# Kernel optimization log

Measured on AMD Instinct MI355X. Metric: run time of the kernel, lower is better.

The kernel has to match this reference:

```python
import jax, jax.numpy as jnp
import numpy as np

# NOTE: the original source calls an undefined selective_scan_fn(x, delta, A_bar, B_bar, C)
# and returns y_proj(y). We implement the standard S6 diagonal selective scan it implies:
#   h_t = A_bar_t * h_{t-1} + B_bar_t * u_t   (elementwise over latent dim, h_0 = 0)
#   y_t = C_t * h_t
# with u = x_proj(x) (the only use of the otherwise-dangling x_proj in the source).

IN_CH = 96
OUT_CH = 96
LATENT = 256
BATCH, H, W = 2, 128, 128


def _linear(x, w, b):
    return x @ w.T + b


def _s6(x, xw, xb, bcw, bcb, dw, db, yw, yb):
    # x: [B, L, Cin]
    u = _linear(x, xw, xb)                      # [B, L, D]
    bc = _linear(x, bcw, bcb)                   # [B, L, 2D]
    delta = _linear(x, dw, db)                  # [B, L, D]
    Bm, Cm = jnp.split(bc, 2, axis=-1)
    A_bar = jnp.exp(-jax.nn.softplus(delta))    # in (0, 1)
    B_bar = (1.0 - A_bar) * Bm
    elems = (A_bar, B_bar * u)

    def combine(c1, c2):
        a1, b1 = c1
        a2, b2 = c2
        return (a1 * a2, a2 * b1 + b2)

    _, h = jax.lax.associative_scan(combine, elems, axis=1)  # parallel scan over L
    y = Cm * h
    return _linear(y, yw, yb)                   # [B, L, D]


def setup_inputs() -> dict:
    key = jax.random.key(0)
    ks = jax.random.split(key, 16)
    s = 0.02
    inp = {
        "x": jax.random.normal(ks[0], (BATCH, IN_CH, H, W), jnp.float32),
        # S6 params (shared across all 4 directional scans, as in the source)
        "xw": jax.random.normal(ks[1], (LATENT, IN_CH), jnp.float32) * s,
        "xb": jnp.zeros((LATENT,), jnp.float32),
        "bcw": jax.random.normal(ks[2], (2 * LATENT, IN_CH), jnp.float32) * s,
        "bcb": jnp.zeros((2 * LATENT,), jnp.float32),
        "dw": jax.random.normal(ks[3], (LATENT, IN_CH), jnp.float32) * s,
        "db": jnp.zeros((LATENT,), jnp.float32),
        "yw": jax.random.normal(ks[4], (LATENT, LATENT), jnp.float32) * s,
        "yb": jnp.zeros((LATENT,), jnp.float32),
        # CrossMerge params
        "mw": jax.random.normal(ks[5], (LATENT, 4 * LATENT), jnp.float32) * s,
        "mb": jnp.zeros((LATENT,), jnp.float32),
        "gw": jax.random.normal(ks[6], (LATENT, 4 * LATENT), jnp.float32) * s,
        "gb": jnp.zeros((LATENT,), jnp.float32),
        "ow": jax.random.normal(ks[7], (OUT_CH, LATENT), jnp.float32) * s,
        "ob": jnp.zeros((OUT_CH,), jnp.float32),
    }
    return inp


def reference(x, xw, xb, bcw, bcb, dw, db, yw, yb, mw, mb, gw, gb, ow, ob):
    B, C, Hh, Ww = x.shape
    # cross_scan: 4 directional flattenings
    s1 = x.transpose(0, 2, 3, 1).reshape(B, Hh * Ww, C)   # 'b c h w -> b (h w) c'
    s2 = x.transpose(0, 3, 2, 1).reshape(B, Ww * Hh, C)   # 'b c h w -> b (w h) c'
    s3 = s1[:, ::-1, :]
    s4 = s2[:, ::-1, :]
    p = (xw, xb, bcw, bcb, dw, db, yw, yb)
    y1 = _s6(s1, *p)
    y2 = _s6(s2, *p)
    y3 = _s6(s3, *p)
    y4 = _s6(s4, *p)
    # CrossMerge
    y_cat = jnp.concatenate([y1, y2, y3, y4], axis=-1)    # [B, L, 4D]
    y_merged = _linear(y_cat, mw, mb)
    gate = jax.nn.sigmoid(_linear(y_cat, gw, gb))
    out = _linear(y_merged * gate, ow, ob)                # [B, L, OUT_CH]
    # 'b (h w) c -> b c h w'
    return out.reshape(B, Hh, Ww, -1).transpose(0, 3, 1, 2)
```

## Files before the change

kernel.cpp:

```cpp
#include <hip/hip_runtime.h>
#include <stdint.h>

#define LL 16384
#define NB 2
#define CIN 96
#define NLAT 256
#define COUT 96

typedef __attribute__((ext_vector_type(8))) short short8v;
typedef __attribute__((ext_vector_type(4))) float float4v;

__device__ __forceinline__ float b2f(unsigned short h) {
    return __uint_as_float(((unsigned int)h) << 16);
}
__device__ __forceinline__ unsigned short f2b(float f) {
    unsigned int u = __float_as_uint(f);
    unsigned int r = (u + 0x7FFFu + ((u >> 16) & 1u)) >> 16;
    return (unsigned short)r;
}

#define GLL16(g, s) __builtin_amdgcn_global_load_lds( \
    (const __attribute__((address_space(1))) unsigned int*)(g), \
    (__attribute__((address_space(3))) unsigned int*)(s), 16, 0, 0)

__global__ __launch_bounds__(256) void k_foldw_part(
    const float* __restrict__ yw, const float* __restrict__ mw, const float* __restrict__ gw,
    float* __restrict__ WF)
{
    __shared__ float At[64][68];
    __shared__ float Bt[64][68];
    int jt = blockIdx.x, nt = blockIdx.y, dzk = blockIdx.z;
    int kc = dzk & 3, dz = dzk >> 2;
    int d = dz & 3, mat = dz >> 2;
    const float* src = mat ? gw : mw;
    int j0 = jt * 64, n0 = nt * 64;
    int tid = threadIdx.x, tx = tid & 15, ty = tid >> 4;
    float acc[4][4] = {};
    int i0 = kc * 64;
    for (int rep = 0; rep < 16; ++rep) {
        int idx = rep * 256 + tid;
        int r = idx >> 6, cq = idx & 63;
        At[r][cq] = yw[(size_t)(i0 + r) * 256 + j0 + cq];
        Bt[cq][r] = src[(size_t)(n0 + r) * 1024 + d * 256 + i0 + cq];
    }
    __syncthreads();
    for (int ii = 0; ii < 64; ++ii) {
        float4 a4 = *(const float4*)(&At[ii][ty * 4]);
        float4 b4 = *(const float4*)(&Bt[ii][tx * 4]);
        float av[4] = {a4.x, a4.y, a4.z, a4.w};
        float bv[4] = {b4.x, b4.y, b4.z, b4.w};
        for (int q = 0; q < 4; ++q)
            for (int p = 0; p < 4; ++p)
                acc[q][p] = fmaf(av[q], bv[p], acc[q][p]);
    }
    float* dst = WF + (size_t)kc * 512 * 1024;
    for (int q = 0; q < 4; ++q) {
        int k = d * 256 + j0 + ty * 4 + q;
        for (int p = 0; p < 4; ++p) {
            int n = n0 + tx * 4 + p;
            dst[(size_t)(mat * 256 + n) * 1024 + k] = acc[q][p];
        }
    }
}

__global__ __launch_bounds__(256) void k_foldsum(
    const float* __restrict__ WF, unsigned short* __restrict__ WBT)
{
    int t = blockIdx.x * 256 + threadIdx.x;
    size_t o = (size_t)t * 4;
    const size_t S = (size_t)512 * 1024;
    float4 s0 = *(const float4*)(WF + o);
    float4 s1 = *(const float4*)(WF + S + o);
    float4 s2 = *(const float4*)(WF + 2 * S + o);
    float4 s3 = *(const float4*)(WF + 3 * S + o);
    unsigned short pk[4];
    pk[0] = f2b(s0.x + s1.x + s2.x + s3.x);
    pk[1] = f2b(s0.y + s1.y + s2.y + s3.y);
    pk[2] = f2b(s0.z + s1.z + s2.z + s3.z);
    pk[3] = f2b(s0.w + s1.w + s2.w + s3.w);
    *(unsigned long long*)(&WBT[o]) = *(const unsigned long long*)pk;
}

__global__ void k_foldbias(const float* __restrict__ mw, const float* __restrict__ gw,
                           const float* __restrict__ mb, const float* __restrict__ gb,
                           const float* __restrict__ yb,
                           float* __restrict__ bm2, float* __restrict__ bg2)
{
    int row = blockIdx.x;
    int lane = threadIdx.x;
    int n = row & 255;
    const float* W = (row < 256) ? mw : gw;
    float s = 0.f;
    for (int k = lane; k < 1024; k += 64)
        s = fmaf(W[(size_t)n * 1024 + k], yb[k & 255], s);
    for (int off = 32; off; off >>= 1) s += __shfl_down(s, off);
    if (lane == 0) {
        if (row < 256) bm2[n] = s + mb[n];
        else           bg2[n] = s + gb[n];
    }
}

__global__ __launch_bounds__(256) void k_xpose(
    const float* __restrict__ x, unsigned short* __restrict__ XT)
{
    int t = threadIdx.x;
    int pl = t & 63;
    int grp = t >> 6;
    int p0 = blockIdx.x * 64;
    int b = p0 >> 14;
    int l = (p0 & (LL - 1)) + pl;
    size_t gp = (size_t)(p0 + pl);
    const float* xr = x + (size_t)b * 96 * LL + l;
    unsigned short* orow = XT + gp * 192;
#pragma unroll
    for (int kk = 0; kk < 3; ++kk) {
        int kq = grp * 3 + kk;
        short8v hi, lo;
#pragma unroll
        for (int c = 0; c < 8; ++c) {
            float v = xr[(size_t)(kq * 8 + c) * LL];
            unsigned short h = f2b(v);
            float r = v - b2f(h);
            hi[c] = (short)h;
            lo[c] = (short)f2b(r);
        }
        *(short8v*)(orow + kq * 8) = hi;
        *(short8v*)(orow + 96 + kq * 8) = lo;
    }
}

__global__ void k_wprep(
    const float* __restrict__ xw, const float* __restrict__ bcw, const float* __restrict__ dw,
    unsigned short* __restrict__ WPT)
{
    int rp = blockIdx.x * 32 + (threadIdx.x >> 3);
    int sub = threadIdx.x & 7;
    int nn16 = rp >> 6, g = (rp >> 4) & 3, ni = rp & 15;
    int n = nn16 * 16 + ni;
    const float* row;
    if (g == 0)      row = xw + (size_t)n * 96;
    else if (g == 1) row = bcw + (size_t)n * 96;
    else if (g == 2) row = bcw + (size_t)(256 + n) * 96;
    else             row = dw + (size_t)n * 96;
    unsigned short* orow = WPT + (size_t)rp * 192;
    for (int kq = sub; kq < 12; kq += 8) {
        short8v hv;
#pragma unroll
        for (int c = 0; c < 8; ++c) hv[c] = (short)f2b(row[kq * 8 + c]);
        *(short8v*)(orow + kq * 8) = hv;
        *(short8v*)(orow + 96 + kq * 8) = hv;
    }
}

__global__ void k_owprep(const float* __restrict__ ow, unsigned short* __restrict__ OWB)
{
    int r = blockIdx.x;
    int lane = threadIdx.x;
    unsigned short pk[4];
    if (r < 96) {
        float4 v = *(const float4*)(ow + (size_t)r * 256 + lane * 4);
        pk[0] = f2b(v.x); pk[1] = f2b(v.y); pk[2] = f2b(v.z); pk[3] = f2b(v.w);
    } else {
        pk[0] = pk[1] = pk[2] = pk[3] = 0;
    }
    *(unsigned long long*)(&OWB[(size_t)r * 256 + lane * 4]) = *(const unsigned long long*)pk;
}

__global__ __launch_bounds__(256) void k_proj_mfma(
    const unsigned short* __restrict__ XT, const unsigned short* __restrict__ WPT,
    const float* __restrict__ xb, const float* __restrict__ bcb, const float* __restrict__ db,
    unsigned int* __restrict__ AB, unsigned short* __restrict__ C)
{
    __shared__ __align__(16) unsigned short smA[128 * 32];
    __shared__ __align__(16) unsigned short smB[128 * 32];
    int tid = threadIdx.x;
    int w = tid >> 6, l = tid & 63;
    int mt = blockIdx.x;
    int bnt = blockIdx.y;
    int p0 = mt * 128;
    int bn0 = bnt * 128;

    int rowA = tid >> 2;
    int chA  = tid & 3;
    int laneRow = l & 15;
    int laneK   = l >> 4;

    float4v acc[2][8];
#pragma unroll
    for (int i = 0; i < 2; ++i)
#pragma unroll
        for (int f = 0; f < 8; ++f) acc[i][f] = (float4v)0.f;

    for (int kt = 0; kt < 6; ++kt) {
        const unsigned short* gA = XT + (size_t)(p0 + rowA) * 192 + kt * 32 + chA * 8;
        const unsigned short* gB = WPT + (size_t)(bn0 + rowA) * 192 + kt * 32 + chA * 8;
        GLL16(gA,            smA + tid * 8);
        GLL16(gA + 64 * 192, smA + 2048 + tid * 8);
        GLL16(gB,            smB + tid * 8);
        GLL16(gB + 64 * 192, smB + 2048 + tid * 8);
        __syncthreads();

        short8v a0 = *(const short8v*)(&smA[(w * 32 + laneRow) * 32 + laneK * 8]);
        short8v a1 = *(const short8v*)(&smA[(w * 32 + 16 + laneRow) * 32 + laneK * 8]);
#pragma unroll
        for (int f = 0; f < 8; ++f) {
            short8v bf_ = *(const short8v*)(&smB[(f * 16 + laneRow) * 32 + laneK * 8]);
            acc[0][f] = __builtin_amdgcn_mfma_f32_16x16x32_bf16(a0, bf_, acc[0][f], 0, 0, 0);
            acc[1][f] = __builtin_amdgcn_mfma_f32_16x16x32_bf16(a1, bf_, acc[1][f], 0, 0, 0);
        }
        __syncthreads();
    }

    int lr = l >> 4, lc = l & 15;
#pragma unroll
    for (int mr = 0; mr < 2; ++mr) {
#pragma unroll
        for (int nn2 = 0; nn2 < 2; ++nn2) {
            int n = (bnt * 2 + nn2) * 16 + lc;
            float xbv = xb[n], bb = bcb[n], cb = bcb[256 + n], dbv = db[n];
#pragma unroll
            for (int q = 0; q < 4; ++q) {
                int p = p0 + w * 32 + mr * 16 + lr * 4 + q;
                float u  = acc[mr][nn2 * 4 + 0][q] + xbv;
                float Bm = acc[mr][nn2 * 4 + 1][q] + bb;
                float Cm = acc[mr][nn2 * 4 + 2][q] + cb;
                float dl = acc[mr][nn2 * 4 + 3][q] + dbv;
                float a  = 1.0f / (1.0f + __expf(dl));
                float bu = (1.0f - a) * Bm * u;
                size_t base = (size_t)p * NLAT + n;
                AB[base] = (unsigned int)f2b(a) | ((unsigned int)f2b(bu) << 16);
                C[base]  = f2b(Cm);
            }
        }
    }
}

__device__ __forceinline__ int src_pos(int d, int t) {
    int s = (d >= 2) ? (LL - 1 - t) : t;
    return (d & 1) ? (((s & 127) << 7) | (s >> 7)) : s;
}

__global__ __launch_bounds__(256) void k_scan1(
    const unsigned int* __restrict__ AB,
    float* __restrict__ AggA, float* __restrict__ AggB)
{
    int n = threadIdx.x;
    int c = blockIdx.x, d = blockIdx.y, b = blockIdx.z;
    float h = 0.f, Ap = 1.f;
    int t0 = c * 256;
#pragma unroll 4
    for (int i = 0; i < 256; ++i) {
        int ls = src_pos(d, t0 + i);
        unsigned int v = AB[((size_t)b * LL + ls) * NLAT + n];
        float a  = __uint_as_float(v << 16);
        float bu = __uint_as_float(v & 0xFFFF0000u);
        h = fmaf(a, h, bu);
        Ap *= a;
    }
    size_t o = (((size_t)b * 4 + d) * 64 + c) * NLAT + n;
    AggA[o] = Ap; AggB[o] = h;
}

__global__ void k_scan2(const float* __restrict__ AggA, const float* __restrict__ AggB,
                        float* __restrict__ Hs)
{
    int n = threadIdx.x;
    int d = blockIdx.x, b = blockIdx.y;
    float h = 0.f;
    for (int c = 0; c < 64; ++c) {
        size_t o = (((size_t)b * 4 + d) * 64 + c) * NLAT + n;
        Hs[o] = h;
        h = fmaf(AggA[o], h, AggB[o]);
    }
}

__global__ __launch_bounds__(256) void k_scan3(
    const unsigned int* __restrict__ AB, const unsigned short* __restrict__ C,
    const float* __restrict__ Hs, unsigned short* __restrict__ ys)
{
    int n = threadIdx.x;
    int c = blockIdx.x, d = blockIdx.y, b = blockIdx.z;
    size_t o = (((size_t)b * 4 + d) * 64 + c) * NLAT + n;
    float h = Hs[o];
    int t0 = c * 256;
    size_t ybase = (((size_t)b * 4 + d) * LL + t0) * NLAT + n;
#pragma unroll 4
    for (int i = 0; i < 256; ++i) {
        int ls = src_pos(d, t0 + i);
        size_t idx = ((size_t)b * LL + ls) * NLAT + n;
        unsigned int v = AB[idx];
        float a  = __uint_as_float(v << 16);
        float bu = __uint_as_float(v & 0xFFFF0000u);
        h = fmaf(a, h, bu);
        float y = b2f(C[idx]) * h;
        ys[ybase + (size_t)i * NLAT] = f2b(y);
    }
}

__global__ __launch_bounds__(256) void k_merge_mfma(
    const unsigned short* __restrict__ ys,
    const unsigned short* __restrict__ WBT,
    const float* __restrict__ bm2, const float* __restrict__ bg2,
    unsigned short* __restrict__ z)
{
    __shared__ __align__(16) unsigned short smA[2 * 128 * 64];
    __shared__ __align__(16) unsigned short smB[2 * 128 * 64];
    int tid = threadIdx.x;
    int w = tid >> 6, l = tid & 63;
    int mt = blockIdx.x;
    int nt = blockIdx.y;
    int p0 = mt * 128;
    int b4 = (p0 >> 14) * 4;
    int l0 = p0 & (LL - 1);
    int n0 = nt * 64;

    int rowS = tid >> 3;
    int cg   = (tid & 7) ^ (rowS & 7);
    int laneRow = l & 15;
    int laneK   = l >> 4;
    int rx8 = (laneRow & 7);

    float4v accM[2][4], accG[2][4];
#pragma unroll
    for (int i = 0; i < 2; ++i)
#pragma unroll
        for (int j = 0; j < 4; ++j) { accM[i][j] = (float4v)0.f; accG[i][j] = (float4v)0.f; }

    auto stage = [&](int kt, int buf) {
        int d = kt >> 2;
        int j0k = (kt & 3) * 64;
        const unsigned short* gAb = ys + (((size_t)(b4 + d)) * LL + l0) * 256 + j0k + cg * 8;
        unsigned short* sA = smA + buf * 8192;
        unsigned short* sB = smB + buf * 8192;
#pragma unroll
        for (int rep = 0; rep < 4; ++rep) {
            GLL16(gAb + (size_t)(rep * 32 + rowS) * 256, sA + rep * 2048 + tid * 8);
        }
#pragma unroll
        for (int rep = 0; rep < 4; ++rep) {
            int rr = rep * 32 + rowS;
            int nrow = (rr < 64) ? (n0 + rr) : (256 + n0 + rr - 64);
            GLL16(WBT + (size_t)nrow * 1024 + kt * 64 + cg * 8, sB + rep * 2048 + tid * 8);
        }
    };

    stage(0, 0);

    int cur = 0;
    for (int kt = 0; kt < 16; ++kt) {
        if (kt < 15) {
            stage(kt + 1, cur ^ 1);
            asm volatile("s_waitcnt vmcnt(8)" ::: "memory");
        } else {
            asm volatile("s_waitcnt vmcnt(0)" ::: "memory");
        }
        __builtin_amdgcn_s_barrier();

        const unsigned short* sA = smA + cur * 8192;
        const unsigned short* sB = smB + cur * 8192;
#pragma unroll
        for (int ksub = 0; ksub < 2; ++ksub) {
            int cxo = ((ksub * 4 + laneK) ^ rx8) * 8;
            short8v a0 = *(const short8v*)(&sA[(w * 32 + laneRow) * 64 + cxo]);
            short8v a1 = *(const short8v*)(&sA[(w * 32 + 16 + laneRow) * 64 + cxo]);
#pragma unroll
            for (int nr = 0; nr < 4; ++nr) {
                short8v bm_ = *(const short8v*)(&sB[(nr * 16 + laneRow) * 64 + cxo]);
                short8v bg_ = *(const short8v*)(&sB[(64 + nr * 16 + laneRow) * 64 + cxo]);
                accM[0][nr] = __builtin_amdgcn_mfma_f32_16x16x32_bf16(a0, bm_, accM[0][nr], 0, 0, 0);
                accM[1][nr] = __builtin_amdgcn_mfma_f32_16x16x32_bf16(a1, bm_, accM[1][nr], 0, 0, 0);
                accG[0][nr] = __builtin_amdgcn_mfma_f32_16x16x32_bf16(a0, bg_, accG[0][nr], 0, 0, 0);
                accG[1][nr] = __builtin_amdgcn_mfma_f32_16x16x32_bf16(a1, bg_, accG[1][nr], 0, 0, 0);
            }
        }
        __builtin_amdgcn_s_barrier();
        cur ^= 1;
    }

    int lr = l >> 4, lc = l & 15;
#pragma unroll
    for (int mr = 0; mr < 2; ++mr) {
#pragma unroll
        for (int nr = 0; nr < 4; ++nr) {
            int n = n0 + nr * 16 + lc;
            float bmv = bm2[n], bgv = bg2[n];
#pragma unroll
            for (int q = 0; q < 4; ++q) {
                int p = p0 + w * 32 + mr * 16 + lr * 4 + q;
                float m = accM[mr][nr][q] + bmv;
                float g = accG[mr][nr][q] + bgv;
                float zv = m / (1.f + __expf(-g));
                z[(size_t)p * NLAT + n] = f2b(zv);
            }
        }
    }
}

__global__ __launch_bounds__(256) void k_out_mfma(
    const unsigned short* __restrict__ z, const unsigned short* __restrict__ OWB,
    const float* __restrict__ ob, float* __restrict__ out)
{
    __shared__ __align__(16) unsigned short smA[128 * 32];
    __shared__ __align__(16) unsigned short smB[128 * 32];
    int tid = threadIdx.x;
    int w = tid >> 6, l = tid & 63;
    int p0 = blockIdx.x * 128;
    int b = p0 >> 14;
    int l0 = p0 & (LL - 1);

    int rowA = tid >> 2;
    int chA  = tid & 3;
    int laneRow = l & 15;
    int laneK   = l >> 4;

    float4v acc[2][6];
#pragma unroll
    for (int i = 0; i < 2; ++i)
#pragma unroll
        for (int f = 0; f < 6; ++f) acc[i][f] = (float4v)0.f;

    for (int kt = 0; kt < 8; ++kt) {
        const unsigned short* gA = z + (size_t)(p0 + rowA) * 256 + kt * 32 + chA * 8;
        const unsigned short* gB = OWB + (size_t)rowA * 256 + kt * 32 + chA * 8;
        GLL16(gA,            smA + tid * 8);
        GLL16(gA + 64 * 256, smA + 2048 + tid * 8);
        GLL16(gB,            smB + tid * 8);
        GLL16(gB + 64 * 256, smB + 2048 + tid * 8);
        __syncthreads();

        short8v a0 = *(const short8v*)(&smA[(w * 32 + laneRow) * 32 + laneK * 8]);
        short8v a1 = *(const short8v*)(&smA[(w * 32 + 16 + laneRow) * 32 + laneK * 8]);
#pragma unroll
        for (int nr = 0; nr < 6; ++nr) {
            short8v bf_ = *(const short8v*)(&smB[(nr * 16 + laneRow) * 32 + laneK * 8]);
            acc[0][nr] = __builtin_amdgcn_mfma_f32_16x16x32_bf16(a0, bf_, acc[0][nr], 0, 0, 0);
            acc[1][nr] = __builtin_amdgcn_mfma_f32_16x16x32_bf16(a1, bf_, acc[1][nr], 0, 0, 0);
        }
        __syncthreads();
    }

    int lr = l >> 4, lc = l & 15;
#pragma unroll
    for (int mr = 0; mr < 2; ++mr) {
#pragma unroll
        for (int nr = 0; nr < 6; ++nr) {
            int c = nr * 16 + lc;
            float obv = ob[c];
            int ll = l0 + w * 32 + mr * 16 + lr * 4;
            float4 v;
            v.x = acc[mr][nr][0] + obv;
            v.y = acc[mr][nr][1] + obv;
            v.z = acc[mr][nr][2] + obv;
            v.w = acc[mr][nr][3] + obv;
            *(float4*)(&out[((size_t)(b * 96 + c)) * LL + ll]) = v;
        }
    }
}

extern "C" void kernel_launch(void* const* d_in, const int* in_sizes, int n_in,
                              void* d_out, int out_size, void* d_ws, size_t ws_size,
                              hipStream_t stream) {
    (void)in_sizes; (void)n_in; (void)out_size; (void)ws_size;
    const float* x   = (const float*)d_in[0];
    const float* xw  = (const float*)d_in[1];
    const float* xb  = (const float*)d_in[2];
    const float* bcw = (const float*)d_in[3];
    const float* bcb = (const float*)d_in[4];
    const float* dw  = (const float*)d_in[5];
    const float* db  = (const float*)d_in[6];
    const float* yw  = (const float*)d_in[7];
    const float* yb  = (const float*)d_in[8];
    const float* mw  = (const float*)d_in[9];
    const float* mb  = (const float*)d_in[10];
    const float* gw  = (const float*)d_in[11];
    const float* gb  = (const float*)d_in[12];
    const float* ow  = (const float*)d_in[13];
    const float* ob  = (const float*)d_in[14];
    float* out = (float*)d_out;

    char* ws = (char*)d_ws;
    size_t off = 0;
    auto alloc = [&](size_t bytes) -> void* {
        void* p = ws + off;
        off += (bytes + 255) & ~(size_t)255;
        return p;
    };
    unsigned int*   AB  = (unsigned int*)  alloc((size_t)NB * LL * NLAT * 4);
    unsigned short* C   = (unsigned short*)alloc((size_t)NB * LL * NLAT * 2);
    unsigned short* YS  = (unsigned short*)alloc((size_t)NB * 4 * LL * NLAT * 2);
    unsigned short* Z   = (unsigned short*)alloc((size_t)NB * LL * NLAT * 2);
    unsigned short* WBT = (unsigned short*)alloc((size_t)512 * 1024 * 2);
    unsigned short* XT  = (unsigned short*)alloc((size_t)NB * LL * 192 * 2);
    unsigned short* WPT = (unsigned short*)alloc((size_t)1024 * 192 * 2);
    unsigned short* OWB = (unsigned short*)alloc((size_t)128 * 256 * 2);
    float* WF   = (float*)alloc((size_t)4 * 512 * 1024 * 4);
    float* BM2  = (float*)alloc(256 * 4);
    float* BG2  = (float*)alloc(256 * 4);
    float* AggA = (float*)alloc((size_t)NB * 4 * 64 * NLAT * 4);
    float* AggB = (float*)alloc((size_t)NB * 4 * 64 * NLAT * 4);
    float* HS   = (float*)alloc((size_t)NB * 4 * 64 * NLAT * 4);

    k_foldw_part<<<dim3(4, 4, 32),  256, 0, stream>>>(yw, mw, gw, WF);
    k_foldsum   <<<512,             256, 0, stream>>>(WF, WBT);
    k_foldbias  <<<512,              64, 0, stream>>>(mw, gw, mb, gb, yb, BM2, BG2);
    k_wprep     <<<32,              256, 0, stream>>>(xw, bcw, dw, WPT);
    k_owprep    <<<128,              64, 0, stream>>>(ow, OWB);
    k_xpose     <<<512,             256, 0, stream>>>(x, XT);
    k_proj_mfma <<<dim3(256, 8),    256, 0, stream>>>(XT, WPT, xb, bcb, db, AB, C);
    k_scan1     <<<dim3(64, 4, NB), 256, 0, stream>>>(AB, AggA, AggB);
    k_scan2     <<<dim3(4, NB),     256, 0, stream>>>(AggA, AggB, HS);
    k_scan3     <<<dim3(64, 4, NB), 256, 0, stream>>>(AB, C, HS, YS);
    k_merge_mfma<<<dim3(256, 4),    256, 0, stream>>>(YS, WBT, BM2, BG2, Z);
    k_out_mfma  <<<256,             256, 0, stream>>>(Z, OWB, ob, out);
}
```

Measured before the change: 195.7 us.

## Retile merge GEMM to 128x128 output per block with 2x2 warp grid

The merge GEMM block tile grows from 128x64 to 128x128 output columns, for both the M and G halves. The four warps are arranged 2x2, each owning a 64x64 sub-tile, and the K step shrinks from 64 to 32 with a matching swizzle. The goal is to raise arithmetic intensity and halve how often the ys activation tile is reloaded across column blocks. The cost is 128 accumulator float4 registers per thread, which may cut occupancy or cause spills. The grid also halves to 512 blocks.

```diff
diff --git a/kernel.cpp b/kernel.cpp
--- a/kernel.cpp
+++ b/kernel.cpp
@@ -303,74 +303,75 @@
     const float* __restrict__ bm2, const float* __restrict__ bg2,
     unsigned short* __restrict__ z)
 {
-    __shared__ __align__(16) unsigned short smA[2 * 128 * 64];
-    __shared__ __align__(16) unsigned short smB[2 * 128 * 64];
+    __shared__ __align__(16) unsigned short smA[2 * 128 * 32];
+    __shared__ __align__(16) unsigned short smB[2 * 256 * 32];
     int tid = threadIdx.x;
     int w = tid >> 6, l = tid & 63;
+    int wm = w >> 1, wn = w & 1;
     int mt = blockIdx.x;
     int nt = blockIdx.y;
     int p0 = mt * 128;
     int b4 = (p0 >> 14) * 4;
     int l0 = p0 & (LL - 1);
-    int n0 = nt * 64;
-
-    int rowS = tid >> 3;
-    int cg   = (tid & 7) ^ (rowS & 7);
+    int n0 = nt * 128;
+
+    int rS = tid >> 2;
+    int cg = (tid & 3) ^ ((rS >> 1) & 3);
     int laneRow = l & 15;
     int laneK   = l >> 4;
-    int rx8 = (laneRow & 7);
-
-    float4v accM[2][4], accG[2][4];
-#pragma unroll
-    for (int i = 0; i < 2; ++i)
+    int rx = (laneRow >> 1) & 3;
+
+    float4v accM[4][4], accG[4][4];
+#pragma unroll
+    for (int i = 0; i < 4; ++i)
 #pragma unroll
         for (int j = 0; j < 4; ++j) { accM[i][j] = (float4v)0.f; accG[i][j] = (float4v)0.f; }
 
     auto stage = [&](int kt, int buf) {
-        int d = kt >> 2;
-        int j0k = (kt & 3) * 64;
+        int d = kt >> 3;
+        int j0k = (kt & 7) * 32;
         const unsigned short* gAb = ys + (((size_t)(b4 + d)) * LL + l0) * 256 + j0k + cg * 8;
-        unsigned short* sA = smA + buf * 8192;
+        unsigned short* sA = smA + buf * 4096;
         unsigned short* sB = smB + buf * 8192;
 #pragma unroll
+        for (int rep = 0; rep < 2; ++rep) {
+            GLL16(gAb + (size_t)(rep * 64 + rS) * 256, sA + rep * 2048 + tid * 8);
+        }
+#pragma unroll
         for (int rep = 0; rep < 4; ++rep) {
-            GLL16(gAb + (size_t)(rep * 32 + rowS) * 256, sA + rep * 2048 + tid * 8);
-        }
-#pragma unroll
-        for (int rep = 0; rep < 4; ++rep) {
-            int rr = rep * 32 + rowS;
-            int nrow = (rr < 64) ? (n0 + rr) : (256 + n0 + rr - 64);
-            GLL16(WBT + (size_t)nrow * 1024 + kt * 64 + cg * 8, sB + rep * 2048 + tid * 8);
+            int rr = rep * 64 + rS;
+            int nrow = (rr < 128) ? (n0 + rr) : (256 + n0 + rr - 128);
+            GLL16(WBT + (size_t)nrow * 1024 + kt * 32 + cg * 8, sB + rep * 2048 + tid * 8);
         }
     };
 
     stage(0, 0);
 
     int cur = 0;
-    for (int kt = 0; kt < 16; ++kt) {
-        if (kt < 15) {
+    for (int kt = 0; kt < 32; ++kt) {
+        if (kt < 31) {
             stage(kt + 1, cur ^ 1);
-            asm volatile("s_waitcnt vmcnt(8)" ::: "memory");
+            asm volatile("s_waitcnt vmcnt(6)" ::: "memory");
         } else {
             asm volatile("s_waitcnt vmcnt(0)" ::: "memory");
         }
         __builtin_amdgcn_s_barrier();
 
-        const unsigned short* sA = smA + cur * 8192;
+        const unsigned short* sA = smA + cur * 4096;
         const unsigned short* sB = smB + cur * 8192;
-#pragma unroll
-        for (int ksub = 0; ksub < 2; ++ksub) {
-            int cxo = ((ksub * 4 + laneK) ^ rx8) * 8;
-            short8v a0 = *(const short8v*)(&sA[(w * 32 + laneRow) * 64 + cxo]);
-            short8v a1 = *(const short8v*)(&sA[(w * 32 + 16 + laneRow) * 64 + cxo]);
-#pragma unroll
-            for (int nr = 0; nr < 4; ++nr) {
-                short8v bm_ = *(const short8v*)(&sB[(nr * 16 + laneRow) * 64 + cxo]);
-                short8v bg_ = *(const short8v*)(&sB[(64 + nr * 16 + laneRow) * 64 + cxo]);
-                accM[0][nr] = __builtin_amdgcn_mfma_f32_16x16x32_bf16(a0, bm_, accM[0][nr], 0, 0, 0);
-                accM[1][nr] = __builtin_amdgcn_mfma_f32_16x16x32_bf16(a1, bm_, accM[1][nr], 0, 0, 0);
-                accG[0][nr] = __builtin_amdgcn_mfma_f32_16x16x32_bf16(a0, bg_, accG[0][nr], 0, 0, 0);
-                accG[1][nr] = __builtin_amdgcn_mfma_f32_16x16x32_bf16(a1, bg_, accG[1][nr], 0, 0, 0);
+        int cxo = (laneK ^ rx) * 8;
+        short8v a[4];
+#pragma unroll
+        for (int mr = 0; mr < 4; ++mr)
+            a[mr] = *(const short8v*)(&sA[(wm * 64 + mr * 16 + laneRow) * 32 + cxo]);
+#pragma unroll
+        for (int nr = 0; nr < 4; ++nr) {
+            short8v bm_ = *(const short8v*)(&sB[(wn * 64 + nr * 16 + laneRow) * 32 + cxo]);
+            short8v bg_ = *(const short8v*)(&sB[(128 + wn * 64 + nr * 16 + laneRow) * 32 + cxo]);
+#pragma unroll
+            for (int mr = 0; mr < 4; ++mr) {
+                accM[mr][nr] = __builtin_amdgcn_mfma_f32_16x16x32_bf16(a[mr], bm_, accM[mr][nr], 0, 0, 0);
+                accG[mr][nr] = __builtin_amdgcn_mfma_f32_16x16x32_bf16(a[mr], bg_, accG[mr][nr], 0, 0, 0);
             }
         }
         __builtin_amdgcn_s_barrier();
@@ -379,14 +380,14 @@
 
     int lr = l >> 4, lc = l & 15;
 #pragma unroll
-    for (int mr = 0; mr < 2; ++mr) {
+    for (int mr = 0; mr < 4; ++mr) {
 #pragma unroll
         for (int nr = 0; nr < 4; ++nr) {
-            int n = n0 + nr * 16 + lc;
+            int n = n0 + wn * 64 + nr * 16 + lc;
             float bmv = bm2[n], bgv = bg2[n];
 #pragma unroll
             for (int q = 0; q < 4; ++q) {
-                int p = p0 + w * 32 + mr * 16 + lr * 4 + q;
+                int p = p0 + wm * 64 + mr * 16 + lr * 4 + q;
                 float m = accM[mr][nr][q] + bmv;
                 float g = accG[mr][nr][q] + bgv;
                 float zv = m / (1.f + __expf(-g));
@@ -510,6 +511,6 @@
     k_scan1     <<<dim3(64, 4, NB), 256, 0, stream>>>(AB, AggA, AggB);
     k_scan2     <<<dim3(4, NB),     256, 0, stream>>>(AggA, AggB, HS);
     k_scan3     <<<dim3(64, 4, NB), 256, 0, stream>>>(AB, C, HS, YS);
-    k_merge_mfma<<<dim3(256, 4),    256, 0, stream>>>(YS, WBT, BM2, BG2, Z);
+    k_merge_mfma<<<dim3(256, 2),    256, 0, stream>>>(YS, WBT, BM2, BG2, Z);
     k_out_mfma  <<<256,             256, 0, stream>>>(Z, OWB, ob, out);
 }
```

New measurement: 191.8 us. 1.02x faster.
